# Kernel tuning notes

Measured on AMD Instinct MI355X. Metric: run time of the kernel, lower is better.

Reference implementation:

```python
import jax, jax.numpy as jnp
import numpy as np

N, E = 50000, 800000
IN, HID, OUT = 128, 128, 64
BN_EPS = 1e-5


def _w(key, fan_in, fan_out):
    return jax.random.normal(key, (fan_in, fan_out), dtype=jnp.float32) / np.sqrt(fan_in)


def setup_inputs() -> dict:
    key = jax.random.key(0)
    ks = jax.random.split(key, 12)
    x = jax.random.normal(ks[0], (N, IN), dtype=jnp.float32)
    src = jax.random.randint(ks[1], (E,), 0, N, dtype=jnp.int32)
    dst = jax.random.randint(ks[2], (E,), 0, N, dtype=jnp.int32)
    eps = jax.random.normal(ks[3], (N, OUT), dtype=jnp.float32)
    return {
        "x": x, "src": src, "dst": dst, "eps": eps,
        # SAGEConv 1: in -> hidden (lin_l has bias, lin_r no bias, mean aggr)
        "W1l": _w(ks[4], IN, HID), "W1r": _w(ks[5], IN, HID), "b1": jnp.zeros((HID,), jnp.float32),
        "g1": jnp.ones((HID,), jnp.float32), "be1": jnp.zeros((HID,), jnp.float32),
        # SAGEConv 2: hidden -> 2*hidden
        "W2l": _w(ks[6], HID, 2 * HID), "W2r": _w(ks[7], HID, 2 * HID), "b2": jnp.zeros((2 * HID,), jnp.float32),
        "g2": jnp.ones((2 * HID,), jnp.float32), "be2": jnp.zeros((2 * HID,), jnp.float32),
        # SAGEConv 3: 2*hidden -> 2*out
        "W3l": _w(ks[8], 2 * HID, 2 * OUT), "W3r": _w(ks[9], 2 * HID, 2 * OUT), "b3": jnp.zeros((2 * OUT,), jnp.float32),
    }


def _sage(h, src, dst, Wl, Wr, b):
    # mean-aggregate source features at destination nodes, then two GEMMs
    msg = jax.ops.segment_sum(h[src], dst, num_segments=N)          # [N, F]
    deg = jax.ops.segment_sum(jnp.ones((src.shape[0],), h.dtype), dst, num_segments=N)
    aggr = msg / jnp.maximum(deg, 1.0)[:, None]
    return aggr @ Wl + h @ Wr + b


def _bn(h, gamma, beta):
    m = jnp.mean(h, axis=0)
    v = jnp.var(h, axis=0)
    return gamma * (h - m) * jax.lax.rsqrt(v + BN_EPS) + beta


def reference(x, src, dst, eps, W1l, W1r, b1, g1, be1, W2l, W2r, b2, g2, be2, W3l, W3r, b3):
    h = jax.nn.relu(_sage(x, src, dst, W1l, W1r, b1))
    h = _bn(h, g1, be1)                       # dropout = identity (eval)
    h = jax.nn.relu(_sage(h, src, dst, W2l, W2r, b2))
    h = _bn(h, g2, be2)
    h = _sage(h, src, dst, W3l, W3r, b3)      # [N, 2*OUT]
    mean, log_std = jnp.split(h, 2, axis=-1)
    z = mean + jnp.exp(log_std) * eps         # reparameterize
    return z
```

## Files before the change

kernel.cpp:

```cpp
#include <hip/hip_runtime.h>
#include <math.h>

#define N_NODES 50000
#define N_EDGES 800000
#define BN_EPS_F 1e-5f
#define SCAN_BS 512
#define SCAN_NB 98
#define GXP 392

typedef unsigned short ushort_t;
typedef unsigned int uint_t;
typedef __attribute__((ext_vector_type(8))) short bf16x8;
typedef __attribute__((ext_vector_type(4))) float f32x4;

static __device__ __forceinline__ float4 ld4(const float* p) {
    return *reinterpret_cast<const float4*>(p);
}
static __device__ __forceinline__ float bf2f(ushort_t u) {
    return __uint_as_float(((uint_t)u) << 16);
}
static __device__ __forceinline__ ushort_t f2b(float f) {
    uint_t u = __float_as_uint(f);
    u += 0x7fffu + ((u >> 16) & 1u);
    return (ushort_t)(u >> 16);
}
static __device__ __forceinline__ void gload16(const void* g, void* l) {
    __builtin_amdgcn_global_load_lds(
        (const __attribute__((address_space(1))) void*)g,
        (__attribute__((address_space(3))) void*)l, 16, 0, 0);
}


__global__ void k_zero_i32(int* __restrict__ p, int n) {
    int i = blockIdx.x * blockDim.x + threadIdx.x;
    if (i < n) p[i] = 0;
}

__global__ void k_pre(const int* __restrict__ dst, int* __restrict__ deg,
                      ushort_t* __restrict__ rank,
                      const float* __restrict__ x, ushort_t* __restrict__ xb,
                      const float* __restrict__ W1l, const float* __restrict__ W1r,
                      const float* __restrict__ W2l, ushort_t* __restrict__ wt1l,
                      ushort_t* __restrict__ wt1r, ushort_t* __restrict__ wt2l) {
    int b = blockIdx.x;
    if (b < 6250) {
        int role = b & 1;
        int id = (b >> 1) * 256 + threadIdx.x;
        if (role == 0) {
            rank[id] = (ushort_t)atomicAdd(&deg[dst[id]], 1);
        } else {
            float4 a = ld4(x + (size_t)id * 8);
            float4 c = ld4(x + (size_t)id * 8 + 4);
            uint_t o0 = (uint_t)f2b(a.x) | ((uint_t)f2b(a.y) << 16);
            uint_t o1 = (uint_t)f2b(a.z) | ((uint_t)f2b(a.w) << 16);
            uint_t o2 = (uint_t)f2b(c.x) | ((uint_t)f2b(c.y) << 16);
            uint_t o3 = (uint_t)f2b(c.z) | ((uint_t)f2b(c.w) << 16);
            *reinterpret_cast<uint4*>(xb + (size_t)id * 8) = make_uint4(o0, o1, o2, o3);
        }
    } else {
        int idx = (b - 6250) * 256 + threadIdx.x;
        if (idx < 16384) {
            int f = idx >> 7, k = idx & 127;
            wt1l[idx] = f2b(W1l[(size_t)k * 128 + f]);
        } else if (idx < 32768) {
            int j = idx - 16384;
            int f = j >> 7, k = j & 127;
            wt1r[j] = f2b(W1r[(size_t)k * 128 + f]);
        } else {
            int j = idx - 32768;
            int f = j >> 7, k = j & 127;
            wt2l[j] = f2b(W2l[(size_t)k * 256 + f]);
        }
    }
}

__global__ void k_scan1(const int* __restrict__ deg, int* __restrict__ offs, int* __restrict__ bsum) {
    __shared__ int sh[SCAN_BS];
    int t = threadIdx.x;
    int g = blockIdx.x * SCAN_BS + t;
    int v = (g < N_NODES) ? deg[g] : 0;
    sh[t] = v;
    __syncthreads();
    for (int off = 1; off < SCAN_BS; off <<= 1) {
        int add = (t >= off) ? sh[t - off] : 0;
        __syncthreads();
        sh[t] += add;
        __syncthreads();
    }
    if (g < N_NODES) offs[g] = sh[t] - v;
    if (t == SCAN_BS - 1) bsum[blockIdx.x] = sh[t];
}

__global__ void k_scan2(int* __restrict__ bsum, int nb) {
    __shared__ int sh[128];
    int t = threadIdx.x;
    int v = (t < nb) ? bsum[t] : 0;
    sh[t] = v;
    __syncthreads();
    for (int off = 1; off < 128; off <<= 1) {
        int add = (t >= off) ? sh[t - off] : 0;
        __syncthreads();
        sh[t] += add;
        __syncthreads();
    }
    if (t < nb) bsum[t] = sh[t] - v;
}

__global__ void k_scan3(const int* __restrict__ deg, int* __restrict__ offs,
                        const int* __restrict__ bsum, float* __restrict__ inv_deg) {
    int g = blockIdx.x * blockDim.x + threadIdx.x;
    if (g < N_NODES) {
        offs[g] += bsum[g / SCAN_BS];
        int d = deg[g];
        inv_deg[g] = 1.0f / (float)(d > 1 ? d : 1);
    }
}

__global__ void k_fill2(const int* __restrict__ src, const int* __restrict__ dst,
                        const int* __restrict__ offs, const ushort_t* __restrict__ rank,
                        ushort_t* __restrict__ eids) {
    int e = blockIdx.x * blockDim.x + threadIdx.x;
    if (e < N_EDGES) eids[offs[dst[e]] + (int)rank[e]] = (ushort_t)src[e];
}


__global__ void k_prep2(const float* __restrict__ W2r, const float* __restrict__ b2,
                        const float* __restrict__ scsh1, ushort_t* __restrict__ wt2r,
                        float* __restrict__ bias2) {
    int bid = blockIdx.x;
    if (bid < 128) {
        int idx = bid * 256 + threadIdx.x;
        int f = idx >> 7, k = idx & 127;
        wt2r[idx] = f2b(scsh1[k] * W2r[(size_t)k * 256 + f]);
    } else {
        int f = threadIdx.x;
        float s = b2[f];
        for (int k = 0; k < 128; ++k) s += scsh1[128 + k] * W2r[(size_t)k * 256 + f];
        bias2[f] = s;
    }
}

__global__ void k_prep3(const float* __restrict__ W3l, const float* __restrict__ W3r,
                        const float* __restrict__ b3, const float* __restrict__ scsh2,
                        ushort_t* __restrict__ wt3l, ushort_t* __restrict__ wt3r,
                        float* __restrict__ bias3l, float* __restrict__ bias3r) {
    int bid = blockIdx.x;
    if (bid < 256) {
        int half = bid >> 7;
        int idx = (bid & 127) * 256 + threadIdx.x;
        int f = idx >> 8, k = idx & 255;
        const float* W = half ? W3r : W3l;
        ushort_t* WT = half ? wt3r : wt3l;
        WT[idx] = f2b(scsh2[k] * W[(size_t)k * 128 + f]);
    } else {
        int t = threadIdx.x;
        int f = t & 127;
        const float* W = (t < 128) ? W3l : W3r;
        float s = (t < 128) ? 0.f : b3[f];
        for (int k = 0; k < 256; ++k) s += scsh2[256 + k] * W[(size_t)k * 128 + f];
        float* out = (t < 128) ? bias3l : bias3r;
        out[f] = s;
    }
}


#define ACCUM8(a) do { \
    acc[0] += bf2f((ushort_t)(a).x); acc[1] += bf2f((ushort_t)((a).x >> 16)); \
    acc[2] += bf2f((ushort_t)(a).y); acc[3] += bf2f((ushort_t)((a).y >> 16)); \
    acc[4] += bf2f((ushort_t)(a).z); acc[5] += bf2f((ushort_t)((a).z >> 16)); \
    acc[6] += bf2f((ushort_t)(a).w); acc[7] += bf2f((ushort_t)((a).w >> 16)); } while (0)

static __device__ __forceinline__ void gather_rows_g(
        const ushort_t* __restrict__ h, const ushort_t* __restrict__ eids,
        int beg, int d, size_t coff, float* acc) {
    int j = 0;
    for (; j + 8 <= d; j += 8) {
        uint4 a[8];
#pragma unroll
        for (int k = 0; k < 8; ++k) {
            int s = eids[beg + j + k];
            a[k] = *reinterpret_cast<const uint4*>(h + (size_t)s * 128 + coff);
        }
#pragma unroll
        for (int k = 0; k < 8; ++k) ACCUM8(a[k]);
    }
    for (; j + 4 <= d; j += 4) {
        uint4 a[4];
#pragma unroll
        for (int k = 0; k < 4; ++k) {
            int s = eids[beg + j + k];
            a[k] = *reinterpret_cast<const uint4*>(h + (size_t)s * 128 + coff);
        }
#pragma unroll
        for (int k = 0; k < 4; ++k) ACCUM8(a[k]);
    }
    for (; j + 2 <= d; j += 2) {
        int s0 = eids[beg + j];
        int s1 = eids[beg + j + 1];
        uint4 a = *reinterpret_cast<const uint4*>(h + (size_t)s0 * 128 + coff);
        uint4 b = *reinterpret_cast<const uint4*>(h + (size_t)s1 * 128 + coff);
        ACCUM8(a); ACCUM8(b);
    }
    if (j < d) {
        int s0 = eids[beg + j];
        uint4 a = *reinterpret_cast<const uint4*>(h + (size_t)s0 * 128 + coff);
        ACCUM8(a);
    }
}

template<int BN>
__global__ __launch_bounds__(256) void k_agg16(
        const ushort_t* __restrict__ h, const ushort_t* __restrict__ eids,
        const int* __restrict__ offs, const int* __restrict__ deg,
        const float* __restrict__ inv_deg, const float* __restrict__ scsh,
        ushort_t* __restrict__ out) {
    const int node = blockIdx.x * 16 + (threadIdx.x >> 4);
    const int lr = threadIdx.x & 15;
    if (node >= N_NODES) return;
    float acc[8];
#pragma unroll
    for (int v = 0; v < 8; ++v) acc[v] = 0.f;
    const int beg = offs[node];
    const int d = deg[node];
    const size_t coff = (size_t)lr * 8;
    gather_rows_g(h, eids, beg, d, coff, acc);

    float sc = inv_deg[node];
    if (BN) {
        float4 sa0 = ld4(&scsh[lr * 8]), sa1 = ld4(&scsh[lr * 8 + 4]);
        float4 sb0 = ld4(&scsh[128 + lr * 8]), sb1 = ld4(&scsh[128 + lr * 8 + 4]);
        if (d > 0) {
            acc[0] = acc[0] * sc * sa0.x + sb0.x; acc[1] = acc[1] * sc * sa0.y + sb0.y;
            acc[2] = acc[2] * sc * sa0.z + sb0.z; acc[3] = acc[3] * sc * sa0.w + sb0.w;
            acc[4] = acc[4] * sc * sa1.x + sb1.x; acc[5] = acc[5] * sc * sa1.y + sb1.y;
            acc[6] = acc[6] * sc * sa1.z + sb1.z; acc[7] = acc[7] * sc * sa1.w + sb1.w;
        } else {
#pragma unroll
            for (int v = 0; v < 8; ++v) acc[v] = 0.f;
        }
    } else {
#pragma unroll
        for (int v = 0; v < 8; ++v) acc[v] *= sc;
    }
    uint4 o;
    o.x = (uint_t)f2b(acc[0]) | ((uint_t)f2b(acc[1]) << 16);
    o.y = (uint_t)f2b(acc[2]) | ((uint_t)f2b(acc[3]) << 16);
    o.z = (uint_t)f2b(acc[4]) | ((uint_t)f2b(acc[5]) << 16);
    o.w = (uint_t)f2b(acc[6]) | ((uint_t)f2b(acc[7]) << 16);
    *reinterpret_cast<uint4*>(out + (size_t)node * 128 + coff) = o;
}

__global__ __launch_bounds__(256) void k_agg_reparam(
        const ushort_t* __restrict__ t3, const ushort_t* __restrict__ eids,
        const int* __restrict__ offs, const int* __restrict__ deg,
        const float* __restrict__ inv_deg, const ushort_t* __restrict__ u,
        const float* __restrict__ eps, float* __restrict__ z) {
    const int node = blockIdx.x * 16 + (threadIdx.x >> 4);
    const int lr = threadIdx.x & 15;
    if (node >= N_NODES) return;
    float acc[8];
#pragma unroll
    for (int v = 0; v < 8; ++v) acc[v] = 0.f;
    const int beg = offs[node];
    const int d = deg[node];
    const size_t coff = (size_t)lr * 8;
    gather_rows_g(t3, eids, beg, d, coff, acc);
    float ls[8];
#pragma unroll
    for (int v = 0; v < 8; ++v) ls[v] = __shfl_down(acc[v], 8);

    if (lr < 8) {
        float sc = inv_deg[node];
        uint4 um4 = *reinterpret_cast<const uint4*>(u + (size_t)node * 128 + lr * 8);
        uint4 ul4 = *reinterpret_cast<const uint4*>(u + (size_t)node * 128 + 64 + lr * 8);
        const float* ep = eps + (size_t)node * 64 + lr * 8;
        float4 e0 = ld4(ep), e1 = ld4(ep + 4);
        float um[8], ul[8];
        um[0] = bf2f((ushort_t)um4.x); um[1] = bf2f((ushort_t)(um4.x >> 16));
        um[2] = bf2f((ushort_t)um4.y); um[3] = bf2f((ushort_t)(um4.y >> 16));
        um[4] = bf2f((ushort_t)um4.z); um[5] = bf2f((ushort_t)(um4.z >> 16));
        um[6] = bf2f((ushort_t)um4.w); um[7] = bf2f((ushort_t)(um4.w >> 16));
        ul[0] = bf2f((ushort_t)ul4.x); ul[1] = bf2f((ushort_t)(ul4.x >> 16));
        ul[2] = bf2f((ushort_t)ul4.y); ul[3] = bf2f((ushort_t)(ul4.y >> 16));
        ul[4] = bf2f((ushort_t)ul4.z); ul[5] = bf2f((ushort_t)(ul4.z >> 16));
        ul[6] = bf2f((ushort_t)ul4.w); ul[7] = bf2f((ushort_t)(ul4.w >> 16));
        float4 o0, o1;
        o0.x = (acc[0] * sc + um[0]) + expf(ls[0] * sc + ul[0]) * e0.x;
        o0.y = (acc[1] * sc + um[1]) + expf(ls[1] * sc + ul[1]) * e0.y;
        o0.z = (acc[2] * sc + um[2]) + expf(ls[2] * sc + ul[2]) * e0.z;
        o0.w = (acc[3] * sc + um[3]) + expf(ls[3] * sc + ul[3]) * e0.w;
        o1.x = (acc[4] * sc + um[4]) + expf(ls[4] * sc + ul[4]) * e1.x;
        o1.y = (acc[5] * sc + um[5]) + expf(ls[5] * sc + ul[5]) * e1.y;
        o1.z = (acc[6] * sc + um[6]) + expf(ls[6] * sc + ul[6]) * e1.z;
        o1.w = (acc[7] * sc + um[7]) + expf(ls[7] * sc + ul[7]) * e1.w;
        float* zp = z + (size_t)node * 64 + lr * 8;
        *reinterpret_cast<float4*>(zp) = o0;
        *reinterpret_cast<float4*>(zp + 4) = o1;
    }
}


template<int RELU, int OUTB, int DUAL, int BIAS, int STATS, int SELY>
__global__ __launch_bounds__(256) void k_gemm_mfma(
        const ushort_t* __restrict__ A1, const ushort_t* __restrict__ A2,
        const ushort_t* __restrict__ B1, const ushort_t* __restrict__ B2,
        const float* __restrict__ bias, void* __restrict__ out,
        int K, int F, float* __restrict__ partials,
        const float* __restrict__ bias2, void* __restrict__ out2) {
    __shared__ __align__(16) short lds[8192];
    const int tid = threadIdx.x;
    const int lane = tid & 63;
    const int w = tid >> 6;
    const int row0 = blockIdx.x * 128;
    const int col0 = SELY ? 0 : blockIdx.y * 128;
    const int wr = (w >> 1) * 64;
    const int wc = (w & 1) * 64;

    const ushort_t* __restrict__ B0 = (SELY && blockIdx.y) ? B2 : B1;
    const float* __restrict__ biasp = (SELY && blockIdx.y) ? bias2 : bias;
    void* __restrict__ outp = (SELY && blockIdx.y) ? out2 : out;

    int rowA[2], slA[2];
#pragma unroll
    for (int p = 0; p < 2; ++p) {
        int c = (p * 4 + w) * 64 + lane;
        int r = c >> 2, sp = c & 3;
        rowA[p] = r;
        slA[p] = sp ^ ((r >> 1) & 3);
    }
    const int q = lane >> 4, lr = lane & 15;
    int aoff[4], boff[4];
#pragma unroll
    for (int f = 0; f < 4; ++f) {
        int ra = wr + f * 16 + lr;
        aoff[f] = ra * 32 + (q ^ ((ra >> 1) & 3)) * 8;
        int rb = wc + f * 16 + lr;
        boff[f] = 4096 + rb * 32 + (q ^ ((rb >> 1) & 3)) * 8;
    }

    f32x4 acc[4][4];
#pragma unroll
    for (int mf = 0; mf < 4; ++mf)
#pragma unroll
        for (int nf = 0; nf < 4; ++nf)
            acc[mf][nf] = (f32x4){0.f, 0.f, 0.f, 0.f};

    for (int m = 0; m < (DUAL ? 2 : 1); ++m) {
        const ushort_t* __restrict__ A = m ? A2 : A1;
        const ushort_t* __restrict__ B = m ? B2 : B0;
        for (int k0 = 0; k0 < K; k0 += 32) {
            __syncthreads();
#pragma unroll
            for (int p = 0; p < 2; ++p) {
                int gr = row0 + rowA[p];
                if (gr > N_NODES - 1) gr = N_NODES - 1;
                gload16(A + (size_t)gr * K + k0 + slA[p] * 8, &lds[(p * 4 + w) * 512]);
                int gc = col0 + rowA[p];
                gload16(B + (size_t)gc * K + k0 + slA[p] * 8, &lds[4096 + (p * 4 + w) * 512]);
            }
            asm volatile("s_waitcnt vmcnt(0)" ::: "memory");
            __syncthreads();
            bf16x8 av[4], bv[4];
#pragma unroll
            for (int f = 0; f < 4; ++f) {
                av[f] = *reinterpret_cast<const bf16x8*>(&lds[aoff[f]]);
                bv[f] = *reinterpret_cast<const bf16x8*>(&lds[boff[f]]);
            }
#pragma unroll
            for (int mf = 0; mf < 4; ++mf)
#pragma unroll
                for (int nf = 0; nf < 4; ++nf)
                    acc[mf][nf] = __builtin_amdgcn_mfma_f32_16x16x32_bf16(
                        av[mf], bv[nf], acc[mf][nf], 0, 0, 0);
        }
    }

    const int orow = row0 + wr + q * 4;
    const int ocol = col0 + wc + lr;
    float s[4], s2[4];
#pragma unroll
    for (int nf = 0; nf < 4; ++nf) { s[nf] = 0.f; s2[nf] = 0.f; }
#pragma unroll
    for (int nf = 0; nf < 4; ++nf) {
        int colg = ocol + nf * 16;
        float bvs = BIAS ? biasp[colg] : 0.f;
#pragma unroll
        for (int mf = 0; mf < 4; ++mf) {
#pragma unroll
            for (int b = 0; b < 4; ++b) {
                int r = orow + mf * 16 + b;
                if (r < N_NODES) {
                    float v = acc[mf][nf][b] + bvs;
                    if (RELU) v = fmaxf(v, 0.f);
                    if (STATS) { s[nf] += v; s2[nf] += v * v; }
                    if (OUTB)
                        ((ushort_t*)outp)[(size_t)r * F + colg] = f2b(v);
                    else
                        ((float*)outp)[(size_t)r * F + colg] = v;
                }
            }
        }
    }

    if constexpr (STATS) {
        __syncthreads();
        float* sdf = (float*)lds;
        const int u = (w >> 1) * 4 + q;
#pragma unroll
        for (int nf = 0; nf < 4; ++nf) {
            int cb = wc + nf * 16 + lr;
            sdf[u * 128 + cb] = s[nf];
            sdf[1024 + u * 128 + cb] = s2[nf];
        }
        __syncthreads();
        if (tid < 128) {
            float ss = 0.f, qq = 0.f;
#pragma unroll
            for (int u2 = 0; u2 < 8; ++u2) {
                ss += sdf[u2 * 128 + tid];
                qq += sdf[1024 + u2 * 128 + tid];
            }
            int cg = col0 + tid;
            partials[(size_t)cg * GXP + blockIdx.x] = ss;
            partials[(size_t)(F + cg) * GXP + blockIdx.x] = qq;
        }
    }
}


template<int F>
__global__ __launch_bounds__(64) void k_bn_scsh(
        const float* __restrict__ partials, const float* __restrict__ gamma,
        const float* __restrict__ beta, float* __restrict__ scsh, int GX) {
    const int c = blockIdx.x;
    const int l = threadIdx.x;
    float s = 0.f, q2 = 0.f;
    for (int g = l; g < GX; g += 64) {
        s += partials[(size_t)c * GXP + g];
        q2 += partials[(size_t)(F + c) * GXP + g];
    }
#pragma unroll
    for (int off = 1; off < 64; off <<= 1) {
        s += __shfl_xor(s, off);
        q2 += __shfl_xor(q2, off);
    }
    if (l == 0) {
        float mean = s * (1.0f / N_NODES);
        float var = q2 * (1.0f / N_NODES) - mean * mean;
        float sc = gamma[c] * rsqrtf(var + BN_EPS_F);
        scsh[c] = sc;
        scsh[F + c] = beta[c] - mean * sc;
    }
}


extern "C" void kernel_launch(void* const* d_in, const int* in_sizes, int n_in,
                              void* d_out, int out_size, void* d_ws, size_t ws_size,
                              hipStream_t stream) {
    (void)in_sizes; (void)n_in; (void)out_size; (void)ws_size;
    const float* x   = (const float*)d_in[0];
    const int*   src = (const int*)d_in[1];
    const int*   dst = (const int*)d_in[2];
    const float* eps = (const float*)d_in[3];
    const float* W1l = (const float*)d_in[4];
    const float* W1r = (const float*)d_in[5];
    const float* b1  = (const float*)d_in[6];
    const float* g1  = (const float*)d_in[7];
    const float* be1 = (const float*)d_in[8];
    const float* W2l = (const float*)d_in[9];
    const float* W2r = (const float*)d_in[10];
    const float* b2  = (const float*)d_in[11];
    const float* g2  = (const float*)d_in[12];
    const float* be2 = (const float*)d_in[13];
    const float* W3l = (const float*)d_in[14];
    const float* W3r = (const float*)d_in[15];
    const float* b3  = (const float*)d_in[16];
    float* z = (float*)d_out;

    char* ws = (char*)d_ws;
    size_t off = 0;
    auto alloc = [&](size_t bytes) -> char* {
        char* p = ws + off;
        off += (bytes + 255) & ~(size_t)255;
        return p;
    };
    int*      deg    = (int*)alloc(N_NODES * 4);
    size_t zero_bytes = off;
    ushort_t* rank   = (ushort_t*)alloc((size_t)N_EDGES * 2);
    ushort_t* eids   = (ushort_t*)alloc((size_t)N_EDGES * 2);
    float*    scshs  = (float*)alloc(1024 * 4);
    float*    biases = (float*)alloc(512 * 4);
    int*      offs   = (int*)alloc(N_NODES * 4);
    int*      bsum   = (int*)alloc(128 * 4);
    float*    invd   = (float*)alloc(N_NODES * 4);
    ushort_t* xb     = (ushort_t*)alloc((size_t)N_NODES * 128 * 2);
    ushort_t* h1b    = (ushort_t*)alloc((size_t)N_NODES * 128 * 2);
    ushort_t* h2b    = (ushort_t*)alloc((size_t)N_NODES * 256 * 2);
    ushort_t* aggrb  = (ushort_t*)alloc((size_t)N_NODES * 256 * 2);
    ushort_t* u3b    = (ushort_t*)alloc((size_t)N_NODES * 128 * 2);
    float*    parts  = (float*)alloc((size_t)512 * GXP * 4);
    ushort_t* wt1l   = (ushort_t*)alloc(128 * 128 * 2);
    ushort_t* wt1r   = (ushort_t*)alloc(128 * 128 * 2);
    ushort_t* wt2l   = (ushort_t*)alloc(256 * 128 * 2);
    ushort_t* wt2r   = (ushort_t*)alloc(256 * 128 * 2);
    ushort_t* wt3l   = (ushort_t*)alloc(128 * 256 * 2);
    ushort_t* wt3r   = (ushort_t*)alloc(128 * 256 * 2);
    ushort_t* t3b    = aggrb;

    float* scsh1  = scshs;
    float* scsh2  = scshs + 256;
    float* bias2  = biases;
    float* bias3l = biases + 256;
    float* bias3r = biases + 384;

    k_zero_i32<<<((int)(zero_bytes / 4) + 255) / 256, 256, 0, stream>>>((int*)ws, (int)(zero_bytes / 4));
    k_pre<<<6506, 256, 0, stream>>>(dst, deg, rank, x, xb, W1l, W1r, W2l, wt1l, wt1r, wt2l);
    k_scan1<<<SCAN_NB, SCAN_BS, 0, stream>>>(deg, offs, bsum);
    k_scan2<<<1, 128, 0, stream>>>(bsum, SCAN_NB);
    k_scan3<<<(N_NODES + 255) / 256, 256, 0, stream>>>(deg, offs, bsum, invd);
    k_fill2<<<(N_EDGES + 255) / 256, 256, 0, stream>>>(src, dst, offs, rank, eids);

    const int AGG_BLKS = N_NODES / 16;
    const int GX = (N_NODES + 127) / 128;

    k_agg16<0><<<AGG_BLKS, 256, 0, stream>>>(xb, eids, offs, deg, invd, nullptr, aggrb);
    k_gemm_mfma<1, 1, 1, 1, 1, 0><<<dim3(GX, 1), 256, 0, stream>>>(aggrb, xb, wt1l, wt1r, b1, h1b, 128, 128, parts, nullptr, nullptr);
    k_bn_scsh<128><<<128, 64, 0, stream>>>(parts, g1, be1, scsh1, GX);

    k_prep2<<<129, 256, 0, stream>>>(W2r, b2, scsh1, wt2r, bias2);
    k_agg16<1><<<AGG_BLKS, 256, 0, stream>>>(h1b, eids, offs, deg, invd, scsh1, aggrb);
    k_gemm_mfma<1, 1, 1, 1, 1, 0><<<dim3(GX, 2), 256, 0, stream>>>(aggrb, h1b, wt2l, wt2r, bias2, h2b, 128, 256, parts, nullptr, nullptr);
    k_bn_scsh<256><<<256, 64, 0, stream>>>(parts, g2, be2, scsh2, GX);

    k_prep3<<<257, 256, 0, stream>>>(W3l, W3r, b3, scsh2, wt3l, wt3r, bias3l, bias3r);
    k_gemm_mfma<0, 1, 0, 1, 0, 1><<<dim3(GX, 2), 256, 0, stream>>>(h2b, nullptr, wt3l, wt3r, bias3l, t3b, 256, 128, nullptr, bias3r, u3b);
    k_agg_reparam<<<AGG_BLKS, 256, 0, stream>>>(t3b, eids, offs, deg, invd, u3b, eps, z);
}
```

Before: 258.1 us.

## Replace LDS-staged MFMA GEMM with direct-load 256x64 tiles and LDS-staged stores

Rewrites the dense GEMM kernels so each wave loads its A rows and B columns directly from global memory into registers, with no LDS staging or per-k-step barriers. Tiles become 256 rows by 64 columns, and the K loop is fully unrolled via a template parameter. Blocks are remapped over a 1D grid in groups of 8 row-tiles per column block to improve L2 reuse. The epilogue now stages bf16 results in LDS and writes coalesced 16-byte stores, and the BN partial layout is adjusted to match. The risk is lost data reuse across waves, since each wave re-reads the B tile, plus redundant global traffic without the shared staging.

```diff
diff --git a/kernel.cpp b/kernel.cpp
--- a/kernel.cpp
+++ b/kernel.cpp
@@ -6,7 +6,8 @@
 #define BN_EPS_F 1e-5f
 #define SCAN_BS 512
 #define SCAN_NB 98
-#define GXP 392
+#define GXR 196
+#define GXP2 200
 
 typedef unsigned short ushort_t;
 typedef unsigned int uint_t;
@@ -23,11 +24,6 @@
     uint_t u = __float_as_uint(f);
     u += 0x7fffu + ((u >> 16) & 1u);
     return (ushort_t)(u >> 16);
-}
-static __device__ __forceinline__ void gload16(const void* g, void* l) {
-    __builtin_amdgcn_global_load_lds(
-        (const __attribute__((address_space(1))) void*)g,
-        (__attribute__((address_space(3))) void*)l, 16, 0, 0);
 }
 
 
@@ -300,42 +296,41 @@
 }
 
 
-template<int RELU, int OUTB, int DUAL, int BIAS, int STATS, int SELY>
-__global__ __launch_bounds__(256) void k_gemm_mfma(
+template<int RELU, int DUAL, int STATS, int SEL3, int K, int YT>
+__global__ __launch_bounds__(256) void k_gemm_direct(
         const ushort_t* __restrict__ A1, const ushort_t* __restrict__ A2,
         const ushort_t* __restrict__ B1, const ushort_t* __restrict__ B2,
-        const float* __restrict__ bias, void* __restrict__ out,
-        int K, int F, float* __restrict__ partials,
-        const float* __restrict__ bias2, void* __restrict__ out2) {
-    __shared__ __align__(16) short lds[8192];
+        const float* __restrict__ bias, ushort_t* __restrict__ out,
+        int F, float* __restrict__ partials,
+        const float* __restrict__ bias2, ushort_t* __restrict__ out2) {
+    const int bid = blockIdx.x;
+    const int grp = bid >> 3;
+    const int y = grp / 25;
+    const int rq = grp - y * 25;
+    const int r = (bid & 7) + (rq << 3);
+    if (r >= GXR) return;
+    const int row0 = r * 256;
+
+    int colblk = y, outsel = 0;
+    if (SEL3) { colblk = y & 1; outsel = y >> 1; }
+    const int col0 = colblk * 64;
+    const ushort_t* __restrict__ Bp = (SEL3 && outsel) ? B2 : B1;
+    const float* __restrict__ biasp = (SEL3 && outsel) ? bias2 : bias;
+    ushort_t* __restrict__ outp = (SEL3 && outsel) ? out2 : out;
+
     const int tid = threadIdx.x;
     const int lane = tid & 63;
     const int w = tid >> 6;
-    const int row0 = blockIdx.x * 128;
-    const int col0 = SELY ? 0 : blockIdx.y * 128;
-    const int wr = (w >> 1) * 64;
-    const int wc = (w & 1) * 64;
-
-    const ushort_t* __restrict__ B0 = (SELY && blockIdx.y) ? B2 : B1;
-    const float* __restrict__ biasp = (SELY && blockIdx.y) ? bias2 : bias;
-    void* __restrict__ outp = (SELY && blockIdx.y) ? out2 : out;
-
-    int rowA[2], slA[2];
-#pragma unroll
-    for (int p = 0; p < 2; ++p) {
-        int c = (p * 4 + w) * 64 + lane;
-        int r = c >> 2, sp = c & 3;
-        rowA[p] = r;
-        slA[p] = sp ^ ((r >> 1) & 3);
-    }
     const int q = lane >> 4, lr = lane & 15;
-    int aoff[4], boff[4];
+    const int wrow = row0 + w * 64;
+
+    int arow[4];
+    const ushort_t* bptr[4];
 #pragma unroll
     for (int f = 0; f < 4; ++f) {
-        int ra = wr + f * 16 + lr;
-        aoff[f] = ra * 32 + (q ^ ((ra >> 1) & 3)) * 8;
-        int rb = wc + f * 16 + lr;
-        boff[f] = 4096 + rb * 32 + (q ^ ((rb >> 1) & 3)) * 8;
+        int rr = wrow + f * 16 + lr;
+        arow[f] = rr < N_NODES ? rr : N_NODES - 1;
+        bptr[f] = Bp + (size_t)(col0 + f * 16 + lr) * K + q * 8;
     }
 
     f32x4 acc[4][4];
@@ -345,26 +340,18 @@
         for (int nf = 0; nf < 4; ++nf)
             acc[mf][nf] = (f32x4){0.f, 0.f, 0.f, 0.f};
 
+#pragma unroll
     for (int m = 0; m < (DUAL ? 2 : 1); ++m) {
         const ushort_t* __restrict__ A = m ? A2 : A1;
-        const ushort_t* __restrict__ B = m ? B2 : B0;
+        const ushort_t* __restrict__ B = m ? B2 : Bp;
+#pragma unroll
         for (int k0 = 0; k0 < K; k0 += 32) {
-            __syncthreads();
-#pragma unroll
-            for (int p = 0; p < 2; ++p) {
-                int gr = row0 + rowA[p];
-                if (gr > N_NODES - 1) gr = N_NODES - 1;
-                gload16(A + (size_t)gr * K + k0 + slA[p] * 8, &lds[(p * 4 + w) * 512]);
-                int gc = col0 + rowA[p];
-                gload16(B + (size_t)gc * K + k0 + slA[p] * 8, &lds[4096 + (p * 4 + w) * 512]);
-            }
-            asm volatile("s_waitcnt vmcnt(0)" ::: "memory");
-            __syncthreads();
             bf16x8 av[4], bv[4];
 #pragma unroll
             for (int f = 0; f < 4; ++f) {
-                av[f] = *reinterpret_cast<const bf16x8*>(&lds[aoff[f]]);
-                bv[f] = *reinterpret_cast<const bf16x8*>(&lds[boff[f]]);
+                av[f] = *reinterpret_cast<const bf16x8*>(A + (size_t)arow[f] * K + k0 + q * 8);
+                bv[f] = SEL3 ? *reinterpret_cast<const bf16x8*>(bptr[f] + k0)
+                             : *reinterpret_cast<const bf16x8*>(B + (size_t)(col0 + f * 16 + lr) * K + k0 + q * 8);
             }
 #pragma unroll
             for (int mf = 0; mf < 4; ++mf)
@@ -375,54 +362,55 @@
         }
     }
 
-    const int orow = row0 + wr + q * 4;
-    const int ocol = col0 + wc + lr;
+    __shared__ __align__(16) short lw[4][64][68];
+    __shared__ float sdf[2][16][64];
+
     float s[4], s2[4];
 #pragma unroll
     for (int nf = 0; nf < 4; ++nf) { s[nf] = 0.f; s2[nf] = 0.f; }
 #pragma unroll
     for (int nf = 0; nf < 4; ++nf) {
-        int colg = ocol + nf * 16;
-        float bvs = BIAS ? biasp[colg] : 0.f;
+        float bvs = biasp[col0 + nf * 16 + lr];
 #pragma unroll
         for (int mf = 0; mf < 4; ++mf) {
 #pragma unroll
             for (int b = 0; b < 4; ++b) {
-                int r = orow + mf * 16 + b;
-                if (r < N_NODES) {
-                    float v = acc[mf][nf][b] + bvs;
-                    if (RELU) v = fmaxf(v, 0.f);
-                    if (STATS) { s[nf] += v; s2[nf] += v * v; }
-                    if (OUTB)
-                        ((ushort_t*)outp)[(size_t)r * F + colg] = f2b(v);
-                    else
-                        ((float*)outp)[(size_t)r * F + colg] = v;
-                }
+                int rrow = mf * 16 + q * 4 + b;
+                float v = acc[mf][nf][b] + bvs;
+                if (RELU) v = fmaxf(v, 0.f);
+                if (STATS && (wrow + rrow) < N_NODES) { s[nf] += v; s2[nf] += v * v; }
+                lw[w][rrow][nf * 16 + lr] = (short)f2b(v);
             }
         }
     }
+#pragma unroll
+    for (int rr = 0; rr < 8; ++rr) {
+        int row = rr * 8 + (lane >> 3);
+        int gr = wrow + row;
+        if (gr < N_NODES) {
+            uint4 vv = *reinterpret_cast<const uint4*>(&lw[w][row][(lane & 7) * 8]);
+            *reinterpret_cast<uint4*>(outp + (size_t)gr * F + col0 + (lane & 7) * 8) = vv;
+        }
+    }
 
     if constexpr (STATS) {
+        const int u = w * 4 + q;
+#pragma unroll
+        for (int nf = 0; nf < 4; ++nf) {
+            sdf[0][u][nf * 16 + lr] = s[nf];
+            sdf[1][u][nf * 16 + lr] = s2[nf];
+        }
         __syncthreads();
-        float* sdf = (float*)lds;
-        const int u = (w >> 1) * 4 + q;
-#pragma unroll
-        for (int nf = 0; nf < 4; ++nf) {
-            int cb = wc + nf * 16 + lr;
-            sdf[u * 128 + cb] = s[nf];
-            sdf[1024 + u * 128 + cb] = s2[nf];
-        }
-        __syncthreads();
-        if (tid < 128) {
+        if (tid < 64) {
             float ss = 0.f, qq = 0.f;
 #pragma unroll
-            for (int u2 = 0; u2 < 8; ++u2) {
-                ss += sdf[u2 * 128 + tid];
-                qq += sdf[1024 + u2 * 128 + tid];
+            for (int u2 = 0; u2 < 16; ++u2) {
+                ss += sdf[0][u2][tid];
+                qq += sdf[1][u2][tid];
             }
             int cg = col0 + tid;
-            partials[(size_t)cg * GXP + blockIdx.x] = ss;
-            partials[(size_t)(F + cg) * GXP + blockIdx.x] = qq;
+            partials[(size_t)cg * GXP2 + r] = ss;
+            partials[(size_t)(F + cg) * GXP2 + r] = qq;
         }
     }
 }
@@ -431,13 +419,13 @@
 template<int F>
 __global__ __launch_bounds__(64) void k_bn_scsh(
         const float* __restrict__ partials, const float* __restrict__ gamma,
-        const float* __restrict__ beta, float* __restrict__ scsh, int GX) {
+        const float* __restrict__ beta, float* __restrict__ scsh) {
     const int c = blockIdx.x;
     const int l = threadIdx.x;
     float s = 0.f, q2 = 0.f;
-    for (int g = l; g < GX; g += 64) {
-        s += partials[(size_t)c * GXP + g];
-        q2 += partials[(size_t)(F + c) * GXP + g];
+    for (int g = l; g < GXR; g += 64) {
+        s += partials[(size_t)c * GXP2 + g];
+        q2 += partials[(size_t)(F + c) * GXP2 + g];
     }
 #pragma unroll
     for (int off = 1; off < 64; off <<= 1) {
@@ -498,7 +486,7 @@
     ushort_t* h2b    = (ushort_t*)alloc((size_t)N_NODES * 256 * 2);
     ushort_t* aggrb  = (ushort_t*)alloc((size_t)N_NODES * 256 * 2);
     ushort_t* u3b    = (ushort_t*)alloc((size_t)N_NODES * 128 * 2);
-    float*    parts  = (float*)alloc((size_t)512 * GXP * 4);
+    float*    parts  = (float*)alloc((size_t)512 * GXP2 * 4);
     ushort_t* wt1l   = (ushort_t*)alloc(128 * 128 * 2);
     ushort_t* wt1r   = (ushort_t*)alloc(128 * 128 * 2);
     ushort_t* wt2l   = (ushort_t*)alloc(256 * 128 * 2);
@@ -521,18 +509,20 @@
     k_fill2<<<(N_EDGES + 255) / 256, 256, 0, stream>>>(src, dst, offs, rank, eids);
 
     const int AGG_BLKS = N_NODES / 16;
-    const int GX = (N_NODES + 127) / 128;
 
     k_agg16<0><<<AGG_BLKS, 256, 0, stream>>>(xb, eids, offs, deg, invd, nullptr, aggrb);
-    k_gemm_mfma<1, 1, 1, 1, 1, 0><<<dim3(GX, 1), 256, 0, stream>>>(aggrb, xb, wt1l, wt1r, b1, h1b, 128, 128, parts, nullptr, nullptr);
-    k_bn_scsh<128><<<128, 64, 0, stream>>>(parts, g1, be1, scsh1, GX);
+    k_gemm_direct<1, 1, 1, 0, 128, 2><<<400, 256, 0, stream>>>(
+        aggrb, xb, wt1l, wt1r, b1, h1b, 128, parts, nullptr, nullptr);
+    k_bn_scsh<128><<<128, 64, 0, stream>>>(parts, g1, be1, scsh1);
 
     k_prep2<<<129, 256, 0, stream>>>(W2r, b2, scsh1, wt2r, bias2);
     k_agg16<1><<<AGG_BLKS, 256, 0, stream>>>(h1b, eids, offs, deg, invd, scsh1, aggrb);
-    k_gemm_mfma<1, 1, 1, 1, 1, 0><<<dim3(GX, 2), 256, 0, stream>>>(aggrb, h1b, wt2l, wt2r, bias2, h2b, 128, 256, parts, nullptr, nullptr);
-    k_bn_scsh<256><<<256, 64, 0, stream>>>(parts, g2, be2, scsh2, GX);
+    k_gemm_direct<1, 1, 1, 0, 128, 4><<<800, 256, 0, stream>>>(
+        aggrb, h1b, wt2l, wt2r, bias2, h2b, 256, parts, nullptr, nullptr);
+    k_bn_scsh<256><<<256, 64, 0, stream>>>(parts, g2, be2, scsh2);
 
     k_prep3<<<257, 256, 0, stream>>>(W3l, W3r, b3, scsh2, wt3l, wt3r, bias3l, bias3r);
-    k_gemm_mfma<0, 1, 0, 1, 0, 1><<<dim3(GX, 2), 256, 0, stream>>>(h2b, nullptr, wt3l, wt3r, bias3l, t3b, 256, 128, nullptr, bias3r, u3b);
+    k_gemm_direct<0, 0, 0, 1, 256, 4><<<800, 256, 0, stream>>>(
+        h2b, nullptr, wt3l, wt3r, bias3l, t3b, 128, nullptr, bias3r, u3b);
     k_agg_reparam<<<AGG_BLKS, 256, 0, stream>>>(t3b, eids, offs, deg, invd, u3b, eps, z);
 }
```

New measurement: 256.3 us. No clear change (-0.7%).

## Double-buffer GEMM LDS tiles, remap block order, and pad degree atomics

Applied to the files above, without the earlier changes.

Each GEMM now uses two LDS buffers, so the global-to-LDS load of the next K tile is issued while MFMAs run on the current one, and there is one barrier per step instead of two waits. Blocks are launched on a 1D grid and remapped into groups of 8 row tiles per column tile, which may change L2 locality. K is now a template parameter. Degree counters are spaced 64 bytes apart to cut atomic contention on shared cache lines, and a compact degree array is written for later kernels. The cost is more LDS per block, which can lower occupancy, plus a larger zeroed workspace region.

```diff
diff --git a/kernel.cpp b/kernel.cpp
--- a/kernel.cpp
+++ b/kernel.cpp
@@ -6,6 +6,8 @@
 #define BN_EPS_F 1e-5f
 #define SCAN_BS 512
 #define SCAN_NB 98
+#define RC 391
+#define RQ 49
 #define GXP 392
 
 typedef unsigned short ushort_t;
@@ -36,7 +38,7 @@
     if (i < n) p[i] = 0;
 }
 
-__global__ void k_pre(const int* __restrict__ dst, int* __restrict__ deg,
+__global__ void k_pre(const int* __restrict__ dst, int* __restrict__ deg2,
                       ushort_t* __restrict__ rank,
                       const float* __restrict__ x, ushort_t* __restrict__ xb,
                       const float* __restrict__ W1l, const float* __restrict__ W1r,
@@ -47,7 +49,7 @@
         int role = b & 1;
         int id = (b >> 1) * 256 + threadIdx.x;
         if (role == 0) {
-            rank[id] = (ushort_t)atomicAdd(&deg[dst[id]], 1);
+            rank[id] = (ushort_t)atomicAdd(&deg2[dst[id] * 16], 1);
         } else {
             float4 a = ld4(x + (size_t)id * 8);
             float4 c = ld4(x + (size_t)id * 8 + 4);
@@ -74,11 +76,11 @@
     }
 }
 
-__global__ void k_scan1(const int* __restrict__ deg, int* __restrict__ offs, int* __restrict__ bsum) {
+__global__ void k_scan1(const int* __restrict__ deg2, int* __restrict__ offs, int* __restrict__ bsum) {
     __shared__ int sh[SCAN_BS];
     int t = threadIdx.x;
     int g = blockIdx.x * SCAN_BS + t;
-    int v = (g < N_NODES) ? deg[g] : 0;
+    int v = (g < N_NODES) ? deg2[g * 16] : 0;
     sh[t] = v;
     __syncthreads();
     for (int off = 1; off < SCAN_BS; off <<= 1) {
@@ -106,12 +108,14 @@
     if (t < nb) bsum[t] = sh[t] - v;
 }
 
-__global__ void k_scan3(const int* __restrict__ deg, int* __restrict__ offs,
-                        const int* __restrict__ bsum, float* __restrict__ inv_deg) {
+__global__ void k_scan3(const int* __restrict__ deg2, int* __restrict__ offs,
+                        const int* __restrict__ bsum, float* __restrict__ inv_deg,
+                        int* __restrict__ degc) {
     int g = blockIdx.x * blockDim.x + threadIdx.x;
     if (g < N_NODES) {
         offs[g] += bsum[g / SCAN_BS];
-        int d = deg[g];
+        int d = deg2[g * 16];
+        degc[g] = d;
         inv_deg[g] = 1.0f / (float)(d > 1 ? d : 1);
     }
 }
@@ -300,33 +304,42 @@
 }
 
 
-template<int RELU, int OUTB, int DUAL, int BIAS, int STATS, int SELY>
-__global__ __launch_bounds__(256) void k_gemm_mfma(
+template<int RELU, int DUAL, int STATS, int SEL3, int K>
+__global__ __launch_bounds__(256) void k_gemm_db(
         const ushort_t* __restrict__ A1, const ushort_t* __restrict__ A2,
         const ushort_t* __restrict__ B1, const ushort_t* __restrict__ B2,
-        const float* __restrict__ bias, void* __restrict__ out,
-        int K, int F, float* __restrict__ partials,
-        const float* __restrict__ bias2, void* __restrict__ out2) {
-    __shared__ __align__(16) short lds[8192];
+        const float* __restrict__ bias, ushort_t* __restrict__ out,
+        int F, float* __restrict__ partials,
+        const float* __restrict__ bias2, ushort_t* __restrict__ out2) {
+    __shared__ __align__(16) short lds[2][8192];
+    const int bid = blockIdx.x;
+    const int grp = bid >> 3;
+    const int y = grp / RQ;
+    const int rq = grp - y * RQ;
+    const int r = (bid & 7) + (rq << 3);
+    if (r >= RC) return;
+    const int row0 = r * 128;
+
+    int colblk = y, outsel = 0;
+    if (SEL3) { colblk = 0; outsel = y; }
+    const int col0 = colblk * 128;
+    const ushort_t* __restrict__ Bp = (SEL3 && outsel) ? B2 : B1;
+    const float* __restrict__ biasp = (SEL3 && outsel) ? bias2 : bias;
+    ushort_t* __restrict__ outp = (SEL3 && outsel) ? out2 : out;
+
     const int tid = threadIdx.x;
     const int lane = tid & 63;
     const int w = tid >> 6;
-    const int row0 = blockIdx.x * 128;
-    const int col0 = SELY ? 0 : blockIdx.y * 128;
     const int wr = (w >> 1) * 64;
     const int wc = (w & 1) * 64;
 
-    const ushort_t* __restrict__ B0 = (SELY && blockIdx.y) ? B2 : B1;
-    const float* __restrict__ biasp = (SELY && blockIdx.y) ? bias2 : bias;
-    void* __restrict__ outp = (SELY && blockIdx.y) ? out2 : out;
-
     int rowA[2], slA[2];
 #pragma unroll
     for (int p = 0; p < 2; ++p) {
         int c = (p * 4 + w) * 64 + lane;
-        int r = c >> 2, sp = c & 3;
-        rowA[p] = r;
-        slA[p] = sp ^ ((r >> 1) & 3);
+        int r_ = c >> 2, sp = c & 3;
+        rowA[p] = r_;
+        slA[p] = sp ^ ((r_ >> 1) & 3);
     }
     const int q = lane >> 4, lr = lane & 15;
     int aoff[4], boff[4];
@@ -345,34 +358,47 @@
         for (int nf = 0; nf < 4; ++nf)
             acc[mf][nf] = (f32x4){0.f, 0.f, 0.f, 0.f};
 
-    for (int m = 0; m < (DUAL ? 2 : 1); ++m) {
-        const ushort_t* __restrict__ A = m ? A2 : A1;
-        const ushort_t* __restrict__ B = m ? B2 : B0;
-        for (int k0 = 0; k0 < K; k0 += 32) {
-            __syncthreads();
-#pragma unroll
-            for (int p = 0; p < 2; ++p) {
-                int gr = row0 + rowA[p];
-                if (gr > N_NODES - 1) gr = N_NODES - 1;
-                gload16(A + (size_t)gr * K + k0 + slA[p] * 8, &lds[(p * 4 + w) * 512]);
-                int gc = col0 + rowA[p];
-                gload16(B + (size_t)gc * K + k0 + slA[p] * 8, &lds[4096 + (p * 4 + w) * 512]);
-            }
-            asm volatile("s_waitcnt vmcnt(0)" ::: "memory");
-            __syncthreads();
-            bf16x8 av[4], bv[4];
-#pragma unroll
-            for (int f = 0; f < 4; ++f) {
-                av[f] = *reinterpret_cast<const bf16x8*>(&lds[aoff[f]]);
-                bv[f] = *reinterpret_cast<const bf16x8*>(&lds[boff[f]]);
-            }
-#pragma unroll
-            for (int mf = 0; mf < 4; ++mf)
-#pragma unroll
-                for (int nf = 0; nf < 4; ++nf)
-                    acc[mf][nf] = __builtin_amdgcn_mfma_f32_16x16x32_bf16(
-                        av[mf], bv[nf], acc[mf][nf], 0, 0, 0);
-        }
+    auto stage = [&](int buf, int t) {
+        const ushort_t* A = A1;
+        const ushort_t* B = SEL3 ? Bp : B1;
+        int k0;
+        if (DUAL) {
+            if (t >= 4) { A = A2; B = B2; }
+            k0 = (t & 3) * 32;
+        } else {
+            k0 = t * 32;
+        }
+        short* base = &lds[buf][0];
+#pragma unroll
+        for (int p = 0; p < 2; ++p) {
+            int gr = row0 + rowA[p];
+            if (gr > N_NODES - 1) gr = N_NODES - 1;
+            gload16(A + (size_t)gr * K + k0 + slA[p] * 8, base + (p * 4 + w) * 512);
+            int gc = col0 + rowA[p];
+            gload16(B + (size_t)gc * K + k0 + slA[p] * 8, base + 4096 + (p * 4 + w) * 512);
+        }
+    };
+
+    constexpr int NT = DUAL ? 8 : (K / 32);
+    stage(0, 0);
+    __syncthreads();
+    int cur = 0;
+    for (int t = 0; t < NT; ++t) {
+        if (t + 1 < NT) stage(cur ^ 1, t + 1);
+        bf16x8 av[4], bv[4];
+#pragma unroll
+        for (int f = 0; f < 4; ++f) {
+            av[f] = *reinterpret_cast<const bf16x8*>(&lds[cur][aoff[f]]);
+            bv[f] = *reinterpret_cast<const bf16x8*>(&lds[cur][boff[f]]);
+        }
+#pragma unroll
+        for (int mf = 0; mf < 4; ++mf)
+#pragma unroll
+            for (int nf = 0; nf < 4; ++nf)
+                acc[mf][nf] = __builtin_amdgcn_mfma_f32_16x16x32_bf16(
+                    av[mf], bv[nf], acc[mf][nf], 0, 0, 0);
+        __syncthreads();
+        cur ^= 1;
     }
 
     const int orow = row0 + wr + q * 4;
@@ -383,20 +409,17 @@
 #pragma unroll
     for (int nf = 0; nf < 4; ++nf) {
         int colg = ocol + nf * 16;
-        float bvs = BIAS ? biasp[colg] : 0.f;
+        float bvs = biasp[colg];
 #pragma unroll
         for (int mf = 0; mf < 4; ++mf) {
 #pragma unroll
             for (int b = 0; b < 4; ++b) {
-                int r = orow + mf * 16 + b;
-                if (r < N_NODES) {
+                int rr = orow + mf * 16 + b;
+                if (rr < N_NODES) {
                     float v = acc[mf][nf][b] + bvs;
                     if (RELU) v = fmaxf(v, 0.f);
                     if (STATS) { s[nf] += v; s2[nf] += v * v; }
-                    if (OUTB)
-                        ((ushort_t*)outp)[(size_t)r * F + colg] = f2b(v);
-                    else
-                        ((float*)outp)[(size_t)r * F + colg] = v;
+                    outp[(size_t)rr * F + colg] = f2b(v);
                 }
             }
         }
@@ -404,7 +427,7 @@
 
     if constexpr (STATS) {
         __syncthreads();
-        float* sdf = (float*)lds;
+        float* sdf = (float*)&lds[0][0];
         const int u = (w >> 1) * 4 + q;
 #pragma unroll
         for (int nf = 0; nf < 4; ++nf) {
@@ -421,8 +444,8 @@
                 qq += sdf[1024 + u2 * 128 + tid];
             }
             int cg = col0 + tid;
-            partials[(size_t)cg * GXP + blockIdx.x] = ss;
-            partials[(size_t)(F + cg) * GXP + blockIdx.x] = qq;
+            partials[(size_t)cg * GXP + r] = ss;
+            partials[(size_t)(F + cg) * GXP + r] = qq;
         }
     }
 }
@@ -431,11 +454,11 @@
 template<int F>
 __global__ __launch_bounds__(64) void k_bn_scsh(
         const float* __restrict__ partials, const float* __restrict__ gamma,
-        const float* __restrict__ beta, float* __restrict__ scsh, int GX) {
+        const float* __restrict__ beta, float* __restrict__ scsh) {
     const int c = blockIdx.x;
     const int l = threadIdx.x;
     float s = 0.f, q2 = 0.f;
-    for (int g = l; g < GX; g += 64) {
+    for (int g = l; g < RC; g += 64) {
         s += partials[(size_t)c * GXP + g];
         q2 += partials[(size_t)(F + c) * GXP + g];
     }
@@ -484,7 +507,7 @@
         off += (bytes + 255) & ~(size_t)255;
         return p;
     };
-    int*      deg    = (int*)alloc(N_NODES * 4);
+    int*      deg2   = (int*)alloc((size_t)N_NODES * 16 * 4);
     size_t zero_bytes = off;
     ushort_t* rank   = (ushort_t*)alloc((size_t)N_EDGES * 2);
     ushort_t* eids   = (ushort_t*)alloc((size_t)N_EDGES * 2);
@@ -492,6 +515,7 @@
     float*    biases = (float*)alloc(512 * 4);
     int*      offs   = (int*)alloc(N_NODES * 4);
     int*      bsum   = (int*)alloc(128 * 4);
+    int*      degc   = (int*)alloc(N_NODES * 4);
     float*    invd   = (float*)alloc(N_NODES * 4);
     ushort_t* xb     = (ushort_t*)alloc((size_t)N_NODES * 128 * 2);
     ushort_t* h1b    = (ushort_t*)alloc((size_t)N_NODES * 128 * 2);
@@ -514,25 +538,28 @@
     float* bias3r = biases + 384;
 
     k_zero_i32<<<((int)(zero_bytes / 4) + 255) / 256, 256, 0, stream>>>((int*)ws, (int)(zero_bytes / 4));
-    k_pre<<<6506, 256, 0, stream>>>(dst, deg, rank, x, xb, W1l, W1r, W2l, wt1l, wt1r, wt2l);
-    k_scan1<<<SCAN_NB, SCAN_BS, 0, stream>>>(deg, offs, bsum);
+    k_pre<<<6506, 256, 0, stream>>>(dst, deg2, rank, x, xb, W1l, W1r, W2l, wt1l, wt1r, wt2l);
+    k_scan1<<<SCAN_NB, SCAN_BS, 0, stream>>>(deg2, offs, bsum);
     k_scan2<<<1, 128, 0, stream>>>(bsum, SCAN_NB);
-    k_scan3<<<(N_NODES + 255) / 256, 256, 0, stream>>>(deg, offs, bsum, invd);
+    k_scan3<<<(N_NODES + 255) / 256, 256, 0, stream>>>(deg2, offs, bsum, invd, degc);
     k_fill2<<<(N_EDGES + 255) / 256, 256, 0, stream>>>(src, dst, offs, rank, eids);
 
     const int AGG_BLKS = N_NODES / 16;
-    const int GX = (N_NODES + 127) / 128;
-
-    k_agg16<0><<<AGG_BLKS, 256, 0, stream>>>(xb, eids, offs, deg, invd, nullptr, aggrb);
-    k_gemm_mfma<1, 1, 1, 1, 1, 0><<<dim3(GX, 1), 256, 0, stream>>>(aggrb, xb, wt1l, wt1r, b1, h1b, 128, 128, parts, nullptr, nullptr);
-    k_bn_scsh<128><<<128, 64, 0, stream>>>(parts, g1, be1, scsh1, GX);
+    const int GEMM_G = 8 * RQ;
+
+    k_agg16<0><<<AGG_BLKS, 256, 0, stream>>>(xb, eids, offs, degc, invd, nullptr, aggrb);
+    k_gemm_db<1, 1, 1, 0, 128><<<GEMM_G, 256, 0, stream>>>(
+        aggrb, xb, wt1l, wt1r, b1, h1b, 128, parts, nullptr, nullptr);
+    k_bn_scsh<128><<<128, 64, 0, stream>>>(parts, g1, be1, scsh1);
 
     k_prep2<<<129, 256, 0, stream>>>(W2r, b2, scsh1, wt2r, bias2);
-    k_agg16<1><<<AGG_BLKS, 256, 0, stream>>>(h1b, eids, offs, deg, invd, scsh1, aggrb);
-    k_gemm_mfma<1, 1, 1, 1, 1, 0><<<dim3(GX, 2), 256, 0, stream>>>(aggrb, h1b, wt2l, wt2r, bias2, h2b, 128, 256, parts, nullptr, nullptr);
-    k_bn_scsh<256><<<256, 64, 0, stream>>>(parts, g2, be2, scsh2, GX);
+    k_agg16<1><<<AGG_BLKS, 256, 0, stream>>>(h1b, eids, offs, degc, invd, scsh1, aggrb);
+    k_gemm_db<1, 1, 1, 0, 128><<<GEMM_G * 2, 256, 0, stream>>>(
+        aggrb, h1b, wt2l, wt2r, bias2, h2b, 256, parts, nullptr, nullptr);
+    k_bn_scsh<256><<<256, 64, 0, stream>>>(parts, g2, be2, scsh2);
 
     k_prep3<<<257, 256, 0, stream>>>(W3l, W3r, b3, scsh2, wt3l, wt3r, bias3l, bias3r);
-    k_gemm_mfma<0, 1, 0, 1, 0, 1><<<dim3(GX, 2), 256, 0, stream>>>(h2b, nullptr, wt3l, wt3r, bias3l, t3b, 256, 128, nullptr, bias3r, u3b);
-    k_agg_reparam<<<AGG_BLKS, 256, 0, stream>>>(t3b, eids, offs, deg, invd, u3b, eps, z);
-}
+    k_gemm_db<0, 0, 0, 1, 256><<<GEMM_G * 2, 256, 0, stream>>>(
+        h2b, nullptr, wt3l, wt3r, bias3l, t3b, 128, nullptr, bias3r, u3b);
+    k_agg_reparam<<<AGG_BLKS, 256, 0, stream>>>(t3b, eids, offs, degc, invd, u3b, eps, z);
+}
```

After: 239.9 us, median of 2. 1.08x faster.
